# Kernel tuning notes

Measured on AMD Instinct MI355X. Metric: run time of the kernel, lower is better.

Reference implementation:

```python
import jax, jax.numpy as jnp
import numpy as np

SCORE_THRESH = 0.25
NMS_THRESH = 0.45
DETECTIONS = 100   # self.detections
K_CAND = 300       # fixed pre-NMS candidate count (jit-friendly stand-in for torch.where filtering)
STRIDES = (8, 16, 32)


def setup_inputs() -> dict:
    key = jax.random.key(0)
    ks = jax.random.split(key, 5)
    pred_p3 = jax.random.normal(ks[0], (16, 80, 80, 3, 85), jnp.float32)
    pred_p4 = jax.random.normal(ks[1], (16, 40, 40, 3, 85), jnp.float32)
    pred_p5 = jax.random.normal(ks[2], (16, 20, 20, 3, 85), jnp.float32)
    anchors = jnp.array([[[10, 13], [16, 30], [33, 23]],
                         [[30, 61], [62, 45], [59, 119]],
                         [[116, 90], [156, 198], [373, 326]]], jnp.float32)
    image_shapes = jnp.full((16, 2), 640, jnp.int32)  # (h, w) per image
    scale_factors = jax.random.uniform(ks[3], (16,), jnp.float32, 0.5, 1.5)
    return {"pred_p3": pred_p3, "pred_p4": pred_p4, "pred_p5": pred_p5,
            "anchors": anchors, "image_shapes": image_shapes,
            "scale_factors": scale_factors, "max_size": 4096}


def _decode_level(p, stride, anchor_wh):
    # p: [B,H,W,A,5+C] already sigmoided
    B, H, W, A, _ = p.shape
    gx = jnp.arange(W, dtype=p.dtype)
    gy = jnp.arange(H, dtype=p.dtype)
    grid = jnp.stack(jnp.meshgrid(gx, gy, indexing='xy'), axis=-1)  # [H,W,2] = (x,y)
    xy = (2.0 * p[..., :2] - 0.5 + grid[None, :, :, None, :]) * stride
    wh = 4.0 * p[..., 2:4] ** 2 * anchor_wh  # anchor_wh: [A,2]
    box = jnp.concatenate([xy, wh], axis=-1).reshape(B, H * W * A, 4)
    obj = p[..., 4].reshape(B, H * W * A)
    cls = p[..., 5:].reshape(B, H * W * A, -1)
    return box, obj, cls


def _pairwise_iou(b):  # b: [K,4] xyxy
    area = (b[:, 2] - b[:, 0]) * (b[:, 3] - b[:, 1])
    lt = jnp.maximum(b[:, None, :2], b[None, :, :2])
    rb = jnp.minimum(b[:, None, 2:], b[None, :, 2:])
    wh = jnp.clip(rb - lt, 0.0)
    inter = wh[..., 0] * wh[..., 1]
    return inter / (area[:, None] + area[None, :] - inter + 1e-9)


def _nms_image(boxes, scores, labels, im_shape, scale, max_size):
    # boxes [K,4], scores [K] sorted desc, labels [K] int
    w = im_shape[1].astype(boxes.dtype)
    h = im_shape[0].astype(boxes.dtype)
    boxes = jnp.stack([jnp.clip(boxes[:, 0], 0.0, w), jnp.clip(boxes[:, 1], 0.0, h),
                       jnp.clip(boxes[:, 2], 0.0, w), jnp.clip(boxes[:, 3], 0.0, h)], axis=1)
    # class-offset boxes (batched_nms)
    bn = jax.lax.stop_gradient(boxes + (labels.astype(boxes.dtype) * max_size)[:, None])
    iou = _pairwise_iou(bn)
    s_ng = jax.lax.stop_gradient(scores)
    K = boxes.shape[0]
    ar = jnp.arange(K)

    def body(i, keep):
        active = keep[i] & (s_ng[i] > SCORE_THRESH)
        return keep & ~((iou[i] > NMS_THRESH) & (ar > i) & active)

    keep = jax.lax.fori_loop(0, K, body, jnp.ones(K, bool))
    final = jnp.where(keep & (s_ng > SCORE_THRESH), scores, 0.0)
    det_s, det_i = jax.lax.top_k(final, DETECTIONS)
    det_b = boxes[det_i] / scale
    det_l = labels[det_i].astype(boxes.dtype)
    return jnp.concatenate([det_b, det_s[:, None], det_l[:, None]], axis=1)  # [D,6]


def reference(pred_p3, pred_p4, pred_p5, anchors, image_shapes, scale_factors, max_size):
    boxes_l, obj_l, cls_l = [], [], []
    for i, (pred, stride) in enumerate(zip((pred_p3, pred_p4, pred_p5), STRIDES)):
        p = jax.nn.sigmoid(pred)
        b, o, c = _decode_level(p, float(stride), anchors[i])
        boxes_l.append(b); obj_l.append(o); cls_l.append(c)
    boxes = jnp.concatenate(boxes_l, axis=1)   # [B,N,4] cxcywh
    obj = jnp.concatenate(obj_l, axis=1)       # [B,N]
    cls = jnp.concatenate(cls_l, axis=1)       # [B,N,C]
    # cxcywh -> xyxy
    cx, cy, ww, hh = boxes[..., 0], boxes[..., 1], boxes[..., 2], boxes[..., 3]
    boxes = jnp.stack([cx - ww / 2, cy - hh / 2, cx + ww / 2, cy + hh / 2], axis=-1)
    B, N, C = cls.shape
    logits = obj[..., None] * cls              # [B,N,C]
    valid = (obj[..., None] > SCORE_THRESH) & (logits > SCORE_THRESH)
    flat = jnp.where(valid, logits, 0.0).reshape(B, N * C)
    vals, idx = jax.lax.top_k(flat, K_CAND)    # sorted desc per image
    aidx = idx // C
    labels = idx % C
    cand_boxes = jnp.take_along_axis(boxes, aidx[..., None], axis=1)  # [B,K,4]
    out = jax.vmap(_nms_image, in_axes=(0, 0, 0, 0, 0, None))(
        cand_boxes, vals, labels, image_shapes, scale_factors, jnp.float32(max_size))
    return out  # [B, DETECTIONS, 6] = (x1,y1,x2,y2,score,label)
```

## Files before the change

### kernel.cpp

```cpp
#include <hip/hip_runtime.h>
#include <cstdint>
#include <cstddef>

#define BATCH 16
#define NCLS 80
#define NANCH 25200
#define G 48
#define NCHUNK 525
#define TOTCH (BATCH * NCHUNK)
#define CPB 4
#define ABINS 512
#define SBINS 1024
#define SCAP 2048
#define SCAP2 4096
#define LCAP 1024
#define KC 300
#define DET 100
#define SCORE_T 0.25f
#define NMS_T 0.45f
#define NBLK 50
#define SPAN 504
#define CNTPAD 16

__device__ __forceinline__ float sg(float x) { return 1.0f / (1.0f + expf(-x)); }

__device__ __forceinline__ const float* anchor_base(const float* p3, const float* p4,
                                                    const float* p5, int b, int n) {
    if (n < 19200) return p3 + ((size_t)b * 19200 + n) * 85;
    if (n < 24000) return p4 + ((size_t)b * 4800 + (n - 19200)) * 85;
    return p5 + ((size_t)b * 1200 + (n - 24000)) * 85;
}

struct Chunk { const float4* p; int outbase; int b; };
__device__ __forceinline__ Chunk chunk_of(int g, const float* p3, const float* p4,
                                          const float* p5) {
    Chunk ck;
    int b = g / NCHUNK, ch = g % NCHUNK;
    const float* src; int a0, lvlN, gbase;
    if (ch < 400)      { src = p3; a0 = ch * G;         lvlN = 19200; gbase = 0; }
    else if (ch < 500) { src = p4; a0 = (ch - 400) * G; lvlN = 4800;  gbase = 19200; }
    else               { src = p5; a0 = (ch - 500) * G; lvlN = 1200;  gbase = 24000; }
    ck.p = (const float4*)(src + ((size_t)b * lvlN + a0) * 85);
    ck.outbase = b * NANCH + gbase + a0;
    ck.b = b;
    return ck;
}

__global__ __launch_bounds__(256) void k_max(const float* __restrict__ p3,
                                             const float* __restrict__ p4,
                                             const float* __restrict__ p5,
                                             float* __restrict__ gmax,
                                             unsigned int* __restrict__ ahist) {
    __shared__ __align__(16) float buf[G * 85];
    __shared__ float pmax[5 * G];
    int tid = threadIdx.x;
    int g0 = blockIdx.x * CPB;
    Chunk cur = chunk_of(g0, p3, p4, p5);
    float4 pre[4];
#pragma unroll
    for (int r = 0; r < 4; r++) {
        int i = tid + r * 256;
        pre[r] = (i < (G * 85 / 4)) ? cur.p[i] : make_float4(0.f, 0.f, 0.f, 0.f);
    }
    for (int it = 0; it < CPB; ++it) {
#pragma unroll
        for (int r = 0; r < 4; r++) {
            int i = tid + r * 256;
            if (i < (G * 85 / 4)) ((float4*)buf)[i] = pre[r];
        }
        Chunk nxt = cur;
        if (it + 1 < CPB) {
            nxt = chunk_of(g0 + it + 1, p3, p4, p5);
#pragma unroll
            for (int r = 0; r < 4; r++) {
                int i = tid + r * 256;
                pre[r] = (i < (G * 85 / 4)) ? nxt.p[i] : make_float4(0.f, 0.f, 0.f, 0.f);
            }
        }
        __syncthreads();
        if (tid < 240) {
            int a = tid % G, part = tid / G;
            const float* base = buf + a * 85 + 5 + part * 16;
            float m = base[0];
#pragma unroll
            for (int k = 1; k < 16; k++) m = fmaxf(m, base[k]);
            pmax[part * G + a] = m;
        }
        __syncthreads();
        if (tid < G) {
            float m = pmax[tid];
#pragma unroll
            for (int p = 1; p < 5; p++) m = fmaxf(m, pmax[p * G + tid]);
            float obj = sg(buf[tid * 85 + 4]);
            float v = 0.0f;
            if (obj > SCORE_T) v = obj * sg(m);
            gmax[cur.outbase + tid] = v;
            if (v > SCORE_T) {
                int bin = (int)((v - SCORE_T) * (ABINS / 0.75f));
                bin = bin < 0 ? 0 : (bin > ABINS - 1 ? ABINS - 1 : bin);
                atomicAdd(&ahist[cur.b * ABINS + bin], 1u);
            }
        }
        __syncthreads();
        cur = nxt;
    }
}

__global__ __launch_bounds__(512) void k_collect(
    const float* __restrict__ p3, const float* __restrict__ p4, const float* __restrict__ p5,
    const float* __restrict__ gmax, const unsigned int* __restrict__ ahist,
    unsigned int* __restrict__ shist, unsigned int* __restrict__ scnt,
    float* __restrict__ ss, unsigned int* __restrict__ sidx) {
    __shared__ unsigned int h[ABINS];
    __shared__ int TaS;
    __shared__ int an[SPAN];
    __shared__ float og[SPAN];
    __shared__ float lss[LCAP];
    __shared__ unsigned int lsi[LCAP];
    __shared__ unsigned int ncand, lcnt, gbase;
    int tid = threadIdx.x;
    int b = blockIdx.x / NBLK;
    int blk = blockIdx.x % NBLK;
    if (tid == 0) { ncand = 0u; TaS = 0; lcnt = 0u; }
    h[tid] = ahist[b * ABINS + tid];
    __syncthreads();
    unsigned int run = h[tid];
    __syncthreads();
    for (int off = 1; off < ABINS; off <<= 1) {
        unsigned int add = (tid + off < ABINS) ? h[tid + off] : 0u;
        __syncthreads();
        run += add;
        h[tid] = run;
        __syncthreads();
    }
    if (run >= KC && (tid == ABINS - 1 || h[tid + 1] < KC)) TaS = tid;
    __syncthreads();
    int Ta = TaS;

    int n0 = blk * SPAN;
    for (int i = tid; i < SPAN; i += 512) {
        int n = n0 + i;
        float v = gmax[(size_t)b * NANCH + n];
        if (v > SCORE_T) {
            int bin = (int)((v - SCORE_T) * (ABINS / 0.75f));
            bin = bin < 0 ? 0 : (bin > ABINS - 1 ? ABINS - 1 : bin);
            if (bin >= Ta) {
                unsigned int p = atomicAdd(&ncand, 1u);
                an[p] = n;
            }
        }
    }
    __syncthreads();
    int M = (int)ncand;
    for (int i = tid; i < M; i += 512) {
        const float* pb = anchor_base(p3, p4, p5, b, an[i]);
        og[i] = sg(pb[4]);
    }
    __syncthreads();
    int twoTa = 2 * Ta;
    for (int idx = tid; idx < M * NCLS; idx += 512) {
        int a = idx / NCLS, c = idx - a * NCLS;
        const float* pb = anchor_base(p3, p4, p5, b, an[a]);
        float s = og[a] * sg(pb[5 + c]);
        if (s > SCORE_T) {
            int bin = (int)((s - SCORE_T) * (SBINS / 0.75f));
            bin = bin < 0 ? 0 : (bin > SBINS - 1 ? SBINS - 1 : bin);
            if (bin >= twoTa) {
                atomicAdd(&shist[b * SBINS + bin], 1u);
                unsigned int p = atomicAdd(&lcnt, 1u);
                if (p < LCAP) {
                    lss[p] = s;
                    lsi[p] = (unsigned int)(an[a] * NCLS + c);
                } else {
                    unsigned int q = atomicAdd(&scnt[b * CNTPAD], 1u);
                    if (q < SCAP2) {
                        ss[(size_t)b * SCAP2 + q] = s;
                        sidx[(size_t)b * SCAP2 + q] = (unsigned int)(an[a] * NCLS + c);
                    }
                }
            }
        }
    }
    __syncthreads();
    unsigned int nl = lcnt < LCAP ? lcnt : LCAP;
    if (tid == 0 && nl > 0) gbase = atomicAdd(&scnt[b * CNTPAD], nl);
    __syncthreads();
    for (unsigned int i = tid; i < nl; i += 512) {
        unsigned int p = gbase + i;
        if (p < SCAP2) {
            ss[(size_t)b * SCAP2 + p] = lss[i];
            sidx[(size_t)b * SCAP2 + p] = lsi[i];
        }
    }
}

struct NmsBuf {
    unsigned long long msk[KC * 5];
    float4 bx[KC];
    int lab[KC];
    float sc2[KC];
    float ar[KC];
    unsigned long long keep[5];
    unsigned int actw[10];
    int wpref[6];
    int order[DET];
    int okept[DET];
};

__global__ __launch_bounds__(1024) void k_img(
    const float* __restrict__ p3, const float* __restrict__ p4, const float* __restrict__ p5,
    const float* __restrict__ anchors, const int* __restrict__ imshapes,
    const float* __restrict__ scalef,
    const unsigned int* __restrict__ shist, const unsigned int* __restrict__ scnt_g,
    const float* __restrict__ ss, const unsigned int* __restrict__ sidx,
    float* __restrict__ out) {
    __shared__ unsigned int hist[SBINS];
    __shared__ __align__(16) NmsBuf u;
    __shared__ float cs[SCAP];
    __shared__ unsigned int ci[SCAP];
    __shared__ float sv[KC];
    __shared__ unsigned int si[KC];
    __shared__ unsigned int wtot[16], wsuf[16];
    __shared__ unsigned int scnt_s;
    __shared__ int TsS;

    int b = blockIdx.x;
    int tid = threadIdx.x;
    int lane = tid & 63, wv = tid >> 6;
    if (tid == 0) { scnt_s = 0u; TsS = 0; }

    unsigned int run = shist[b * SBINS + tid];
#pragma unroll
    for (int off = 1; off < 64; off <<= 1) {
        unsigned int v = __shfl_down(run, off, 64);
        if (lane + off < 64) run += v;
    }
    if (lane == 0) wtot[wv] = run;
    __syncthreads();
    if (wv == 0) {
        unsigned int r = (lane < 16) ? wtot[lane] : 0u;
#pragma unroll
        for (int off = 1; off < 16; off <<= 1) {
            unsigned int v = __shfl_down(r, off, 64);
            if (lane + off < 16) r += v;
        }
        if (lane < 16) wsuf[lane] = r;
    }
    __syncthreads();
    unsigned int suf = run + ((wv < 15) ? wsuf[wv + 1] : 0u);
    hist[tid] = suf;
    __syncthreads();
    if (suf >= KC && (tid == SBINS - 1 || hist[tid + 1] < KC)) TsS = tid;
    __syncthreads();
    int Ts = TsS;

    unsigned int total = scnt_g[b * CNTPAD];
    int navail = (int)(total < SCAP2 ? total : SCAP2);
    for (int i = tid; i < navail; i += 1024) {
        float s = ss[(size_t)b * SCAP2 + i];
        int bin = (int)((s - SCORE_T) * (SBINS / 0.75f));
        bin = bin < 0 ? 0 : (bin > SBINS - 1 ? SBINS - 1 : bin);
        if (bin >= Ts) {
            unsigned int pos = atomicAdd(&scnt_s, 1u);
            if (pos < SCAP) { cs[pos] = s; ci[pos] = sidx[(size_t)b * SCAP2 + i]; }
        }
    }
    __syncthreads();
    int nc = (int)(scnt_s < SCAP ? scnt_s : SCAP);

    if (tid < KC) { sv[tid] = 0.f; si[tid] = 0xffffffffu; }
    __syncthreads();
    for (int i = tid; i < nc; i += 1024) {
        float s = cs[i];
        unsigned int ii = ci[i];
        int r = 0;
        for (int j = 0; j < nc; j++) {
            float sj = cs[j];
            unsigned int ij = ci[j];
            if (sj > s || (sj == s && ij < ii)) r++;
        }
        if (r < KC) { sv[r] = s; si[r] = ii; }
    }
    __syncthreads();
    int valid = nc < KC ? nc : KC;

    if (tid < KC) {
        int i = tid;
        if (i < valid) {
            unsigned int fi = si[i];
            int n = (int)(fi / NCLS), c = (int)(fi % NCLS);
            int lvl = (n < 19200) ? 0 : (n < 24000 ? 1 : 2);
            const int offl[3] = {0, 19200, 24000};
            const int Wl[3] = {80, 40, 20};
            const int cntl[3] = {19200, 4800, 1200};
            const float strl[3] = {8.f, 16.f, 32.f};
            const float* pp = lvl == 0 ? p3 : (lvl == 1 ? p4 : p5);
            int nl = n - offl[lvl];
            int a = nl % 3, cell = nl / 3;
            int gx = cell % Wl[lvl], gy = cell / Wl[lvl];
            const float* pb = pp + ((size_t)b * cntl[lvl] + nl) * 85;
            float s0 = sg(pb[0]), s1 = sg(pb[1]), s2 = sg(pb[2]), s3 = sg(pb[3]);
            float stride = strl[lvl];
            float aw = anchors[(lvl * 3 + a) * 2 + 0];
            float ah = anchors[(lvl * 3 + a) * 2 + 1];
            float cx = (2.0f * s0 - 0.5f + (float)gx) * stride;
            float cy = (2.0f * s1 - 0.5f + (float)gy) * stride;
            float bw = 4.0f * s2 * s2 * aw;
            float bh = 4.0f * s3 * s3 * ah;
            float hf = (float)imshapes[b * 2 + 0];
            float wf = (float)imshapes[b * 2 + 1];
            float x1 = cx - bw / 2.0f, y1 = cy - bh / 2.0f;
            float x2 = cx + bw / 2.0f, y2 = cy + bh / 2.0f;
            x1 = fminf(fmaxf(x1, 0.f), wf);
            y1 = fminf(fmaxf(y1, 0.f), hf);
            x2 = fminf(fmaxf(x2, 0.f), wf);
            y2 = fminf(fmaxf(y2, 0.f), hf);
            u.bx[i] = make_float4(x1, y1, x2, y2);
            u.lab[i] = c;
            u.sc2[i] = sv[i];
            u.ar[i] = (x2 - x1) * (y2 - y1);
        } else {
            u.bx[i] = make_float4(0, 0, 0, 0);
            u.lab[i] = -1 - i;
            u.sc2[i] = 0.f;
            u.ar[i] = 0.f;
        }
    }
    __syncthreads();

    if (tid < 10) u.actw[tid] = 0u;
    for (int t = tid; t < KC * 5; t += 1024) {
        int i = t / 5, w = t % 5;
        float4 bi = u.bx[i];
        int li = u.lab[i];
        float ai = u.ar[i];
        unsigned long long m = 0ull;
        for (int tb = 0; tb < 64; tb++) {
            int j = w * 64 + tb;
            if (j < KC && j > i && u.lab[j] == li) {
                float4 bj = u.bx[j];
                float ltx = fmaxf(bi.x, bj.x), lty = fmaxf(bi.y, bj.y);
                float rbx = fminf(bi.z, bj.z), rby = fminf(bi.w, bj.w);
                float iw = fmaxf(rbx - ltx, 0.f), ih = fmaxf(rby - lty, 0.f);
                float inter = iw * ih;
                float iou = inter / (ai + u.ar[j] - inter + 1e-9f);
                if (iou > NMS_T) m |= (1ull << tb);
            }
        }
        u.msk[t] = m;
    }
    __syncthreads();

    for (int i = tid; i < KC; i += 1024) {
        unsigned long long nz = u.msk[i * 5] | u.msk[i * 5 + 1] | u.msk[i * 5 + 2] |
                                u.msk[i * 5 + 3] | u.msk[i * 5 + 4];
        if (nz) atomicOr(&u.actw[i >> 5], 1u << (i & 31));
    }
    __syncthreads();
    if (tid == 0) {
        u.keep[0] = u.keep[1] = u.keep[2] = u.keep[3] = u.keep[4] = ~0ull;
        for (int w = 0; w < 10; w++) {
            unsigned int mw = u.actw[w];
            while (mw) {
                int bpos = __ffs(mw) - 1;
                mw &= mw - 1;
                int i = w * 32 + bpos;
                if ((u.keep[i >> 6] >> (i & 63)) & 1ull) {
#pragma unroll
                    for (int r = 0; r < 5; r++) u.keep[r] &= ~u.msk[i * 5 + r];
                }
            }
        }
        int s = 0;
        for (int w = 0; w < 5; w++) {
            unsigned long long kw = u.keep[w];
            if (w == 4) kw &= (1ull << 44) - 1ull;
            u.wpref[w] = s;
            s += (int)__popcll(kw);
        }
        u.wpref[5] = s;
    }
    __syncthreads();

    if (tid < KC) {
        int w = tid >> 6, bp = tid & 63;
        unsigned long long kw = u.keep[w];
        bool kept = (kw >> bp) & 1ull;
        int r = u.wpref[w] + (int)__popcll(kw & ((1ull << bp) - 1ull));
        if (kept) {
            if (r < DET) { u.order[r] = tid; u.okept[r] = 1; }
        } else {
            int nr = u.wpref[5] + (tid - r);
            if (nr < DET) { u.order[nr] = tid; u.okept[nr] = 0; }
        }
    }
    __syncthreads();

    if (tid < DET) {
        int o = u.order[tid];
        float scale = scalef[b];
        float4 bb = u.bx[o];
        float s = (u.okept[tid] && o < valid) ? u.sc2[o] : 0.f;
        float lb = (o < valid) ? (float)u.lab[o] : 0.f;
        float* po = out + ((size_t)b * DET + tid) * 6;
        po[0] = bb.x / scale;
        po[1] = bb.y / scale;
        po[2] = bb.z / scale;
        po[3] = bb.w / scale;
        po[4] = s;
        po[5] = lb;
    }
}

extern "C" void kernel_launch(void* const* d_in, const int* in_sizes, int n_in,
                              void* d_out, int out_size, void* d_ws, size_t ws_size,
                              hipStream_t stream) {
    const float* p3 = (const float*)d_in[0];
    const float* p4 = (const float*)d_in[1];
    const float* p5 = (const float*)d_in[2];
    const float* anchors = (const float*)d_in[3];
    const int* imshapes = (const int*)d_in[4];
    const float* scalef = (const float*)d_in[5];
    float* out = (float*)d_out;

    char* ws = (char*)d_ws;
    float* gmax = (float*)ws;
    unsigned int* ahist = (unsigned int*)(ws + 1612800);
    unsigned int* shist = (unsigned int*)(ws + 1612800 + 32768);
    unsigned int* scnt  = (unsigned int*)(ws + 1612800 + 32768 + 65536);
    float* ss           = (float*)(ws + 1612800 + 32768 + 65536 + 1024);
    unsigned int* sidx  = (unsigned int*)(ws + 1612800 + 32768 + 65536 + 1024 + 262144);

    hipMemsetAsync(ws + 1612800, 0, 32768 + 65536 + 1024, stream);

    k_max<<<TOTCH / CPB, 256, 0, stream>>>(p3, p4, p5, gmax, ahist);
    k_collect<<<BATCH * NBLK, 512, 0, stream>>>(p3, p4, p5, gmax, ahist, shist, scnt, ss, sidx);
    k_img<<<BATCH, 1024, 0, stream>>>(p3, p4, p5, anchors, imshapes, scalef,
                                      shist, scnt, ss, sidx, out);
}
```

Before: 227.4 us.

## Double-buffer k_max chunks, batch-align blocks, and use wave-shuffle suffix scan

k_max now uses two shared-memory buffers, so the register prefetch of chunk t+2 and the shared store of chunk t+1 happen in the same barrier interval as the reduction on chunk t. This removes one barrier per chunk and overlaps global loads with compute. Each block now handles 7 chunks within a single image (75 blocks per image), so the batch index is fixed per block. The histogram suffix scan in k_collect is replaced by a wave-level shuffle scan plus a small cross-wave pass, cutting the many barrier-separated shared-memory scan steps. The cost is more shared memory per block in k_max and fewer blocks (1200 instead of 2100), which may reduce latency hiding.

```diff
diff --git a/kernel.cpp b/kernel.cpp
--- a/kernel.cpp
+++ b/kernel.cpp
@@ -7,8 +7,8 @@
 #define NANCH 25200
 #define G 48
 #define NCHUNK 525
-#define TOTCH (BATCH * NCHUNK)
-#define CPB 4
+#define CPB 7
+#define NBMAX 75
 #define ABINS 512
 #define SBINS 1024
 #define SCAP 2048
@@ -51,36 +51,40 @@
                                              const float* __restrict__ p5,
                                              float* __restrict__ gmax,
                                              unsigned int* __restrict__ ahist) {
-    __shared__ __align__(16) float buf[G * 85];
+    __shared__ __align__(16) float buf[2][G * 85];
     __shared__ float pmax[5 * G];
     int tid = threadIdx.x;
-    int g0 = blockIdx.x * CPB;
-    Chunk cur = chunk_of(g0, p3, p4, p5);
+    int b = blockIdx.x / NBMAX;
+    int j = blockIdx.x % NBMAX;
+    int g0 = b * NCHUNK + j * CPB;
+
     float4 pre[4];
+    Chunk c0 = chunk_of(g0, p3, p4, p5);
 #pragma unroll
     for (int r = 0; r < 4; r++) {
         int i = tid + r * 256;
-        pre[r] = (i < (G * 85 / 4)) ? cur.p[i] : make_float4(0.f, 0.f, 0.f, 0.f);
-    }
-    for (int it = 0; it < CPB; ++it) {
+        pre[r] = (i < (G * 85 / 4)) ? c0.p[i] : make_float4(0.f, 0.f, 0.f, 0.f);
+    }
+#pragma unroll
+    for (int r = 0; r < 4; r++) {
+        int i = tid + r * 256;
+        if (i < (G * 85 / 4)) ((float4*)buf[0])[i] = pre[r];
+    }
+    {
+        Chunk c1 = chunk_of(g0 + 1, p3, p4, p5);
 #pragma unroll
         for (int r = 0; r < 4; r++) {
             int i = tid + r * 256;
-            if (i < (G * 85 / 4)) ((float4*)buf)[i] = pre[r];
-        }
-        Chunk nxt = cur;
-        if (it + 1 < CPB) {
-            nxt = chunk_of(g0 + it + 1, p3, p4, p5);
-#pragma unroll
-            for (int r = 0; r < 4; r++) {
-                int i = tid + r * 256;
-                pre[r] = (i < (G * 85 / 4)) ? nxt.p[i] : make_float4(0.f, 0.f, 0.f, 0.f);
-            }
-        }
-        __syncthreads();
+            pre[r] = (i < (G * 85 / 4)) ? c1.p[i] : make_float4(0.f, 0.f, 0.f, 0.f);
+        }
+    }
+    __syncthreads();
+
+    for (int t = 0; t < CPB; ++t) {
+        const float* cur = buf[t & 1];
         if (tid < 240) {
             int a = tid % G, part = tid / G;
-            const float* base = buf + a * 85 + 5 + part * 16;
+            const float* base = cur + a * 85 + 5 + part * 16;
             float m = base[0];
 #pragma unroll
             for (int k = 1; k < 16; k++) m = fmaxf(m, base[k]);
@@ -88,21 +92,36 @@
         }
         __syncthreads();
         if (tid < G) {
+            Chunk me = chunk_of(g0 + t, p3, p4, p5);
             float m = pmax[tid];
 #pragma unroll
             for (int p = 1; p < 5; p++) m = fmaxf(m, pmax[p * G + tid]);
-            float obj = sg(buf[tid * 85 + 4]);
+            float obj = sg(cur[tid * 85 + 4]);
             float v = 0.0f;
             if (obj > SCORE_T) v = obj * sg(m);
-            gmax[cur.outbase + tid] = v;
+            gmax[me.outbase + tid] = v;
             if (v > SCORE_T) {
                 int bin = (int)((v - SCORE_T) * (ABINS / 0.75f));
                 bin = bin < 0 ? 0 : (bin > ABINS - 1 ? ABINS - 1 : bin);
-                atomicAdd(&ahist[cur.b * ABINS + bin], 1u);
+                atomicAdd(&ahist[b * ABINS + bin], 1u);
+            }
+        }
+        if (t + 1 < CPB) {
+#pragma unroll
+            for (int r = 0; r < 4; r++) {
+                int i = tid + r * 256;
+                if (i < (G * 85 / 4)) ((float4*)buf[(t + 1) & 1])[i] = pre[r];
+            }
+            if (t + 2 < CPB) {
+                Chunk cn = chunk_of(g0 + t + 2, p3, p4, p5);
+#pragma unroll
+                for (int r = 0; r < 4; r++) {
+                    int i = tid + r * 256;
+                    pre[r] = (i < (G * 85 / 4)) ? cn.p[i] : make_float4(0.f, 0.f, 0.f, 0.f);
+                }
             }
         }
         __syncthreads();
-        cur = nxt;
     }
 }
 
@@ -112,6 +131,7 @@
     unsigned int* __restrict__ shist, unsigned int* __restrict__ scnt,
     float* __restrict__ ss, unsigned int* __restrict__ sidx) {
     __shared__ unsigned int h[ABINS];
+    __shared__ unsigned int wtot[8], wsuf[8];
     __shared__ int TaS;
     __shared__ int an[SPAN];
     __shared__ float og[SPAN];
@@ -119,21 +139,33 @@
     __shared__ unsigned int lsi[LCAP];
     __shared__ unsigned int ncand, lcnt, gbase;
     int tid = threadIdx.x;
+    int lane = tid & 63, wv = tid >> 6;
     int b = blockIdx.x / NBLK;
     int blk = blockIdx.x % NBLK;
     if (tid == 0) { ncand = 0u; TaS = 0; lcnt = 0u; }
-    h[tid] = ahist[b * ABINS + tid];
-    __syncthreads();
-    unsigned int run = h[tid];
-    __syncthreads();
-    for (int off = 1; off < ABINS; off <<= 1) {
-        unsigned int add = (tid + off < ABINS) ? h[tid + off] : 0u;
-        __syncthreads();
-        run += add;
-        h[tid] = run;
-        __syncthreads();
-    }
-    if (run >= KC && (tid == ABINS - 1 || h[tid + 1] < KC)) TaS = tid;
+
+    unsigned int run = ahist[b * ABINS + tid];
+#pragma unroll
+    for (int off = 1; off < 64; off <<= 1) {
+        unsigned int v = __shfl_down(run, off, 64);
+        if (lane + off < 64) run += v;
+    }
+    if (lane == 0) wtot[wv] = run;
+    __syncthreads();
+    if (wv == 0) {
+        unsigned int r = (lane < 8) ? wtot[lane] : 0u;
+#pragma unroll
+        for (int off = 1; off < 8; off <<= 1) {
+            unsigned int v = __shfl_down(r, off, 64);
+            if (lane + off < 8) r += v;
+        }
+        if (lane < 8) wsuf[lane] = r;
+    }
+    __syncthreads();
+    unsigned int suf = run + ((wv < 7) ? wsuf[wv + 1] : 0u);
+    h[tid] = suf;
+    __syncthreads();
+    if (suf >= KC && (tid == ABINS - 1 || h[tid + 1] < KC)) TaS = tid;
     __syncthreads();
     int Ta = TaS;
 
@@ -433,7 +465,7 @@
 
     hipMemsetAsync(ws + 1612800, 0, 32768 + 65536 + 1024, stream);
 
-    k_max<<<TOTCH / CPB, 256, 0, stream>>>(p3, p4, p5, gmax, ahist);
+    k_max<<<BATCH * NBMAX, 256, 0, stream>>>(p3, p4, p5, gmax, ahist);
     k_collect<<<BATCH * NBLK, 512, 0, stream>>>(p3, p4, p5, gmax, ahist, shist, scnt, ss, sidx);
     k_img<<<BATCH, 1024, 0, stream>>>(p3, p4, p5, anchors, imshapes, scalef,
                                       shist, scnt, ss, sidx, out);
```

Result: no change. 230.0 us (+1.1%).
